# Performance work log

Measured on AMD Instinct MI355X. Metric: run time of the kernel, lower is better.

The kernel has to match this reference:

```python
import jax, jax.numpy as jnp
import numpy as np

B, T1, T2 = 2, 1024, 512
D_MODEL, N_HEAD, D_HEAD = 1024, 16, 64
SCALE = 1.0 / D_HEAD ** 0.5
EPS = 1e-5


def _skew(qe):
    # qe: [B, H, T, 2T-1] -> [B, H, T, T] via Transformer-XL pad/reshape trick
    b, h, t, x = qe.shape
    qe = jnp.pad(qe, ((0, 0), (0, 0), (0, 0), (0, 1))).reshape(b, h, 2 * t * t)
    qe = jnp.pad(qe, ((0, 0), (0, 0), (0, t - 1))).reshape(b, h, t + 1, 2 * t - 1)
    return qe[:, :, :t, -t:]


def setup_inputs() -> dict:
    key = jax.random.key(0)
    ks = jax.random.split(key, 12)
    s = 0.02
    return {
        "Q": jax.random.normal(ks[0], (B, T1, D_MODEL), jnp.float32),
        "K": jax.random.normal(ks[1], (B, T1, D_MODEL), jnp.float32),
        "V": jax.random.normal(ks[2], (B, T1, D_MODEL), jnp.float32),
        "lookup_table": jax.random.normal(ks[3], (2 * T1 - 1, D_HEAD), jnp.float32) * s,
        "valid_frames": jnp.sort(jax.random.randint(ks[4], (T2,), 0, T1)),
        "mask": jax.random.bernoulli(ks[5], 0.1, (B, N_HEAD, T1, T2)),
        "Wq": jax.random.normal(ks[6], (D_MODEL, N_HEAD * D_HEAD), jnp.float32) * s,
        "Wk": jax.random.normal(ks[7], (D_MODEL, N_HEAD * D_HEAD), jnp.float32) * s,
        "Wv": jax.random.normal(ks[8], (D_MODEL, N_HEAD * D_HEAD), jnp.float32) * s,
        "Wo": jax.random.normal(ks[9], (N_HEAD * D_HEAD, D_MODEL), jnp.float32) * s,
        "bo": jnp.zeros((D_MODEL,), jnp.float32),
        "ln_g": jnp.ones((D_MODEL,), jnp.float32),
        "ln_b": jnp.zeros((D_MODEL,), jnp.float32),
    }


def reference(Q, K, V, lookup_table, valid_frames, mask, Wq, Wk, Wv, Wo, bo, ln_g, ln_b):
    # gather valid KV frames (raw inputs, before projection)
    K = K[:, valid_frames]  # [B, T2, D]
    V = V[:, valid_frames]
    # pre-layernorm on Q only
    mu = jnp.mean(Q, axis=-1, keepdims=True)
    var = jnp.var(Q, axis=-1, keepdims=True)
    Qn = (Q - mu) * jax.lax.rsqrt(var + EPS) * ln_g + ln_b
    # projections -> [B, H, T, d_head]
    q = (Qn @ Wq).reshape(B, T1, N_HEAD, D_HEAD).transpose(0, 2, 1, 3)
    k = (K @ Wk).reshape(B, T2, N_HEAD, D_HEAD).transpose(0, 2, 1, 3)
    v = (V @ Wv).reshape(B, T2, N_HEAD, D_HEAD).transpose(0, 2, 1, 3)
    # content score + skewed relative-position score
    score = jnp.einsum("bhqd,bhkd->bhqk", q, k)  # [B,H,T1,T2]
    rel = jnp.einsum("bhqd,xd->bhqx", q, lookup_table)  # [B,H,T1,2T1-1]
    rel = _skew(rel)[:, :, :, valid_frames]  # [B,H,T1,T2]
    score = (score + rel) * SCALE
    score = jnp.where(mask, -jnp.finfo(score.dtype).max, score)
    attn = jax.nn.softmax(score, axis=-1)
    ctx = jnp.einsum("bhqk,bhkd->bhqd", attn, v)
    ctx = ctx.transpose(0, 2, 1, 3).reshape(B, T1, N_HEAD * D_HEAD)
    out = ctx @ Wo + bo  # dropout is identity at inference
    return out + ctx  # pre_layernorm=True branch
```

## Files before the change

### kernel.cpp

```cpp
#include <hip/hip_runtime.h>
#include <stdint.h>
#include <stddef.h>

typedef __attribute__((ext_vector_type(8))) short s16x8;
typedef __attribute__((ext_vector_type(4))) short s16x4;
typedef __attribute__((ext_vector_type(4))) float f32x4;

#define MFMA(a,b,c) __builtin_amdgcn_mfma_f32_16x16x32_bf16((a),(b),(c),0,0,0)

static __device__ __forceinline__ unsigned short f2b(float f){
  unsigned int b = __float_as_uint(f);
  b = (b + 0x7FFFu + ((b>>16)&1u)) >> 16;
  return (unsigned short)b;
}
static __device__ __forceinline__ float b2f(unsigned short u){
  return __uint_as_float(((unsigned int)u)<<16);
}


__global__ __launch_bounds__(256) void k_mask(const unsigned char* __restrict__ m,
    unsigned int* __restrict__ MB){
  const int t = threadIdx.x;
  const size_t g0 = (size_t)blockIdx.x*16;
  __shared__ int cnt1, cnt23;
  if(t==0){ cnt1=0; cnt23=0; }
  __syncthreads();
  const uint4* bp = (const uint4*)(m + g0*512);
  int l1=0,l23=0;
  #pragma unroll
  for(int i=0;i<2;i++){
    uint4 v = bp[t + i*256];
    unsigned int ws[4] = {v.x,v.y,v.z,v.w};
    #pragma unroll
    for(int j=0;j<4;j++){
      if((ws[j]>>8)&0xFFu) l1++;
      if(ws[j]>>16)        l23++;
    }
  }
  #pragma unroll
  for(int o=1;o<64;o<<=1){ l1 += __shfl_xor(l1,o); l23 += __shfl_xor(l23,o); }
  if((t&63)==0){ atomicAdd(&cnt1,l1); atomicAdd(&cnt23,l23); }
  __syncthreads();
  const int flag = cnt1 ? 1 : (cnt23 ? 2 : 0);

  const int rl = t>>4, f = t&15;
  const size_t base = (g0 + rl)*512 + f;
  unsigned int word = 0;
  if(flag==0){
    const int* p = (const int*)m;
    #pragma unroll
    for(int i=0;i<32;i++) word |= (p[base+i*16]!=0 ? 1u:0u) << i;
  } else if(flag==1){
    #pragma unroll
    for(int i=0;i<32;i++) word |= (m[base+i*16]!=0 ? 1u:0u) << i;
  } else {
    const float* p = (const float*)m;
    #pragma unroll
    for(int i=0;i<32;i++) word |= (p[base+i*16]!=0.f ? 1u:0u) << i;
  }
  MB[((size_t)blockIdx.x*4 + (t>>6))*64 + f*4 + (rl&3)] = word;
}

__global__ __launch_bounds__(256) void k_prep(
    const float* __restrict__ Q, const float* __restrict__ g, const float* __restrict__ be,
    unsigned short* __restrict__ Qn,
    const float* __restrict__ K, const float* __restrict__ V, const int* __restrict__ vf,
    unsigned short* __restrict__ Kg, unsigned short* __restrict__ Vg,
    const float* __restrict__ L, unsigned short* __restrict__ Lb,
    const float* __restrict__ W0, const float* __restrict__ W1,
    const float* __restrict__ W2, const float* __restrict__ W3,
    unsigned short* __restrict__ D0, unsigned short* __restrict__ D1,
    unsigned short* __restrict__ D2, unsigned short* __restrict__ D3){
  __shared__ float tile[64][65];
  __shared__ float red[8];
  const int bid = blockIdx.x, t = threadIdx.x;
  if(bid < 2048){
    const float4* xp = (const float4*)(Q + (size_t)bid*1024);
    float4 v = xp[t];
    float s  = v.x+v.y+v.z+v.w;
    float s2 = v.x*v.x+v.y*v.y+v.z*v.z+v.w*v.w;
    #pragma unroll
    for(int o=1;o<64;o<<=1){ s += __shfl_xor(s,o); s2 += __shfl_xor(s2,o); }
    int w = t>>6, l = t&63;
    if(l==0){ red[w]=s; red[4+w]=s2; }
    __syncthreads();
    s  = red[0]+red[1]+red[2]+red[3];
    s2 = red[4]+red[5]+red[6]+red[7];
    float mu = s*(1.f/1024.f);
    float var = s2*(1.f/1024.f) - mu*mu;
    float rs = rsqrtf(var + 1e-5f);
    float4 gv = ((const float4*)g)[t];
    float4 bv = ((const float4*)be)[t];
    ushort4 o4;
    o4.x = f2b((v.x-mu)*rs*gv.x + bv.x);
    o4.y = f2b((v.y-mu)*rs*gv.y + bv.y);
    o4.z = f2b((v.z-mu)*rs*gv.z + bv.z);
    o4.w = f2b((v.w-mu)*rs*gv.w + bv.w);
    ((ushort4*)(Qn + (size_t)bid*1024))[t] = o4;
  } else if(bid < 4096){
    int row = bid - 2048;
    int isV = row>>10, r = row&1023;
    int b = r>>9, jj = r&511;
    const float* src = (isV? V : K) + ((size_t)(b*1024 + vf[jj]))*1024;
    unsigned short* dst = (isV? Vg : Kg) + (size_t)r*1024;
    float4 v = ((const float4*)src)[t];
    ushort4 o; o.x=f2b(v.x); o.y=f2b(v.y); o.z=f2b(v.z); o.w=f2b(v.w);
    ((ushort4*)dst)[t] = o;
  } else if(bid < 4608){
    int i = (bid-4096)*256 + t;
    if(i < 2047*64) Lb[i] = f2b(L[i]);
  } else {
    int idx = bid - 4608;
    int z = idx>>8, rem = idx&255;
    int k0 = (rem&15)*64, n0 = (rem>>4)*64;
    const float* S = z==0?W0: z==1?W1: z==2?W2:W3;
    unsigned short* D = z==0?D0: z==1?D1: z==2?D2:D3;
    int tr = t>>6, tc = t&63;
    #pragma unroll
    for(int it=0;it<16;it++){ int r = it*4+tr; tile[r][tc] = S[(size_t)(k0+r)*1024 + n0+tc]; }
    __syncthreads();
    #pragma unroll
    for(int it=0;it<16;it++){ int r = it*4+tr; D[(size_t)(n0+r)*1024 + k0+tc] = f2b(tile[tc][r]); }
  }
}

__global__ __launch_bounds__(256) void k_proj(
    const short* __restrict__ QN, const short* __restrict__ WQT,
    const short* __restrict__ KG, const short* __restrict__ WKT,
    const short* __restrict__ WVT, const short* __restrict__ VG,
    unsigned short* __restrict__ QB, unsigned short* __restrict__ KB,
    unsigned short* __restrict__ VT){
  __shared__ __align__(16) short Ab[128*32];
  __shared__ __align__(16) short Bb[128*32];
  int bid = blockIdx.x;
  int mode, bx;
  if(bid<128){ mode=0; bx=bid>>3; }
  else if(bid<192){ mode=1; bx=(bid-128)>>3; }
  else { mode=2; bx=(bid-192)>>3; }
  int by = bid&7;
  const short* A  = mode==0? QN : mode==1? KG : WVT;
  const short* Bt = mode==0? WQT: mode==1? WKT: VG;

  const int t = threadIdx.x;
  const int w = t>>6, l = t&63;
  const int wr = w>>1, wc = w&1;
  const int fl15 = l&15, fl4 = l>>4;
  const size_t m0 = (size_t)bx*128, n0 = (size_t)by*128;
  const int srow = t>>2, scb = t&3;
  const int sg = scb ^ ((srow>>1)&3);
  const short* Ap = A + (m0+srow)*1024 + 8*sg;
  const short* Bp = Bt + (n0+srow)*1024 + 8*sg;

  f32x4 acc[4][4];
  const f32x4 zero = {0.f,0.f,0.f,0.f};
  #pragma unroll
  for(int m=0;m<4;m++)
    #pragma unroll
    for(int n=0;n<4;n++) acc[m][n] = zero;

  for(int k0=0;k0<1024;k0+=32){
    s16x8 a0 = *(const s16x8*)(Ap + k0);
    s16x8 a1 = *(const s16x8*)(Ap + 64*1024 + k0);
    s16x8 b0 = *(const s16x8*)(Bp + k0);
    s16x8 b1 = *(const s16x8*)(Bp + 64*1024 + k0);
    __syncthreads();
    *(s16x8*)(Ab + srow*32 + scb*8)      = a0;
    *(s16x8*)(Ab + (64+srow)*32 + scb*8) = a1;
    *(s16x8*)(Bb + srow*32 + scb*8)      = b0;
    *(s16x8*)(Bb + (64+srow)*32 + scb*8) = b1;
    __syncthreads();
    s16x8 af[4], bff[4];
    #pragma unroll
    for(int m=0;m<4;m++){
      int row = wr*64 + m*16 + fl15;
      int gg = fl4 ^ ((row>>1)&3);
      af[m] = *(const s16x8*)(Ab + row*32 + gg*8);
    }
    #pragma unroll
    for(int n=0;n<4;n++){
      int row = wc*64 + n*16 + fl15;
      int gg = fl4 ^ ((row>>1)&3);
      bff[n] = *(const s16x8*)(Bb + row*32 + gg*8);
    }
    #pragma unroll
    for(int m=0;m<4;m++)
      #pragma unroll
      for(int n=0;n<4;n++)
        acc[m][n] = MFMA(af[m], bff[n], acc[m][n]);
  }

  #pragma unroll
  for(int m=0;m<4;m++){
    #pragma unroll
    for(int n=0;n<4;n++){
      int mgb = (int)m0 + wr*64 + m*16 + 4*fl4;
      int ng  = (int)n0 + wc*64 + n*16 + fl15;
      #pragma unroll
      for(int p=0;p<4;p++){
        int mg = mgb + p;
        float v = acc[m][n][p];
        if(mode==0){ int b=mg>>10, i=mg&1023, h=ng>>6, d=ng&63;
          QB[((size_t)((b*16+h)*1024+i))*64 + d] = f2b(v); }
        else if(mode==1){ int b=mg>>9, jj=mg&511, h=ng>>6, d=ng&63;
          KB[((size_t)((b*16+h)*512+jj))*64 + d] = f2b(v); }
        else { int h=mg>>6, d=mg&63, b=ng>>9, jj=ng&511;
          VT[((size_t)((b*16+h)*64+d))*512 + jj] = f2b(v); }
      }
    }
  }
}

__global__ __launch_bounds__(256) void k_gemmO(
    const short* __restrict__ A, const short* __restrict__ Bt,
    float* __restrict__ out, const float* __restrict__ bo,
    const float* __restrict__ ctxf){
  __shared__ __align__(16) short Ab[128*32];
  __shared__ __align__(16) short Bb[128*32];
  const int t = threadIdx.x;
  const int w = t>>6, l = t&63;
  const int wr = w>>1, wc = w&1;
  const int fl15 = l&15, fl4 = l>>4;
  const size_t m0 = (size_t)blockIdx.x*128, n0 = (size_t)blockIdx.y*128;
  const int srow = t>>2, scb = t&3;
  const int sg = scb ^ ((srow>>1)&3);
  const short* Ap = A + (m0+srow)*1024 + 8*sg;
  const short* Bp = Bt + (n0+srow)*1024 + 8*sg;

  f32x4 acc[4][4];
  const f32x4 zero = {0.f,0.f,0.f,0.f};
  #pragma unroll
  for(int m=0;m<4;m++)
    #pragma unroll
    for(int n=0;n<4;n++) acc[m][n] = zero;

  for(int k0=0;k0<1024;k0+=32){
    s16x8 a0 = *(const s16x8*)(Ap + k0);
    s16x8 a1 = *(const s16x8*)(Ap + 64*1024 + k0);
    s16x8 b0 = *(const s16x8*)(Bp + k0);
    s16x8 b1 = *(const s16x8*)(Bp + 64*1024 + k0);
    __syncthreads();
    *(s16x8*)(Ab + srow*32 + scb*8)      = a0;
    *(s16x8*)(Ab + (64+srow)*32 + scb*8) = a1;
    *(s16x8*)(Bb + srow*32 + scb*8)      = b0;
    *(s16x8*)(Bb + (64+srow)*32 + scb*8) = b1;
    __syncthreads();
    s16x8 af[4], bff[4];
    #pragma unroll
    for(int m=0;m<4;m++){
      int row = wr*64 + m*16 + fl15;
      int gg = fl4 ^ ((row>>1)&3);
      af[m] = *(const s16x8*)(Ab + row*32 + gg*8);
    }
    #pragma unroll
    for(int n=0;n<4;n++){
      int row = wc*64 + n*16 + fl15;
      int gg = fl4 ^ ((row>>1)&3);
      bff[n] = *(const s16x8*)(Bb + row*32 + gg*8);
    }
    #pragma unroll
    for(int m=0;m<4;m++)
      #pragma unroll
      for(int n=0;n<4;n++)
        acc[m][n] = MFMA(af[m], bff[n], acc[m][n]);
  }

  #pragma unroll
  for(int m=0;m<4;m++){
    #pragma unroll
    for(int n=0;n<4;n++){
      int mgb = (int)m0 + wr*64 + m*16 + 4*fl4;
      int ng  = (int)n0 + wc*64 + n*16 + fl15;
      #pragma unroll
      for(int p=0;p<4;p++){
        int mg = mgb + p;
        size_t idx = (size_t)mg*1024 + ng;
        out[idx] = acc[m][n][p] + bo[ng] + ctxf[idx];
      }
    }
  }
}

#define RCH 256
#define RGS 288
__global__ __launch_bounds__(256) void k_rel(const short* __restrict__ qb,
    const short* __restrict__ lbf, const int* __restrict__ vf,
    unsigned short* __restrict__ relg){
  __shared__ __align__(16) short Gs[4][RGS*16];
  __shared__ int vfs[512];
  const int t=threadIdx.x, w=t>>6, l=t&63, fl15=l&15, fl4=l>>4;
  const int bh = blockIdx.x >> 6;
  const int qg = blockIdx.x & 63;
  const int qw = qg*16;
  for(int i=t;i<512;i+=256) vfs[i]=vf[i];
  __syncthreads();
  const int x0  = 1008 + vfs[0] - qw;
  const int xcw = x0 + w*RCH;
  const short* qp = qb + ((size_t)(bh*1024 + qw + fl15))*64 + 8*fl4;
  s16x8 qa0 = *(const s16x8*)qp;
  s16x8 qa1 = *(const s16x8*)(qp+32);
  short* Gw = &Gs[w][0];
  const f32x4 zero = {0.f,0.f,0.f,0.f};

  #pragma unroll 4
  for(int tt=0;tt<17;tt++){
    int xr = xcw + tt*16 + fl15; if(xr>2046) xr = 2046;
    const short* lp = lbf + (size_t)xr*64 + 8*fl4;
    s16x8 b0 = *(const s16x8*)lp;
    s16x8 b1 = *(const s16x8*)(lp+32);
    f32x4 a = zero;
    a = MFMA(qa0,b0,a); a = MFMA(qa1,b1,a);
    int cb = tt*16 + fl15 + 4*fl4;
    #pragma unroll
    for(int p=0;p<4;p++) Gw[(cb+p)*16 + 4*fl4 + p] = (short)f2b(a[p]);
  }

  unsigned short* rb = relg + ((size_t)(bh*64+qg))*32*256 + l*4;
  #pragma unroll 4
  for(int tt=0;tt<32;tt++){
    int jj = tt*16 + fl15;
    int o  = vfs[jj] - vfs[0] - RCH*w;
    if(o>=0 && o<RCH){
      s16x4 v4 = *(const s16x4*)(Gw + (o+15)*16 + 4*fl4);
      *(s16x4*)(rb + (size_t)tt*256) = v4;
    }
  }
}

__global__ __launch_bounds__(256,2) void k_attn(const short* __restrict__ qb,
    const short* __restrict__ kb, const short* __restrict__ vt,
    const short* __restrict__ relg, const unsigned int* __restrict__ MB,
    unsigned short* __restrict__ ctxb, float* __restrict__ ctxf){
  __shared__ __align__(16) short PB[4][1024];
  const int t=threadIdx.x, w=t>>6, l=t&63, fl15=l&15, fl4=l>>4;
  const int bh = blockIdx.y;
  const int qt = blockIdx.x;
  const int qw = qt*64 + w*16;
  const int qg = qt*4 + w;
  short* Pw = &PB[w][0];

  const int rowgrp = bh*256 + qt*16 + w*4 + fl4;
  uint4 mv = ((const uint4*)MB)[rowgrp*16 + fl15];
  unsigned int mbits[4] = {mv.x, mv.y, mv.z, mv.w};

  const short* qp = qb + ((size_t)(bh*1024 + qw + fl15))*64 + 8*fl4;
  s16x8 qa0 = *(const s16x8*)qp;
  s16x8 qa1 = *(const s16x8*)(qp+32);

  const short* kp_row = kb + ((size_t)(bh*512 + fl15))*64 + 8*fl4;
  const short* rp     = relg + ((size_t)(bh*64+qg))*32*256 + l*4;
  const short* vp[4];
  #pragma unroll
  for(int dt=0;dt<4;dt++) vp[dt] = vt + ((size_t)(bh*64 + dt*16 + fl15))*512 + 8*fl4;

  const f32x4 zero = {0.f,0.f,0.f,0.f};
  f32x4 facc[4];
  #pragma unroll
  for(int dt=0;dt<4;dt++) facc[dt] = zero;
  float m_run[4] = {-1e30f,-1e30f,-1e30f,-1e30f};
  float ps[4]    = {0.f,0.f,0.f,0.f};

  s16x8 kf[2][8];
  s16x4 rf[2][4];
  #pragma unroll
  for(int tl=0;tl<4;tl++){
    const short* ka = kp_row + (size_t)tl*1024;
    kf[0][2*tl]   = *(const s16x8*)ka;
    kf[0][2*tl+1] = *(const s16x8*)(ka+32);
    rf[0][tl]     = *(const s16x4*)(rp + tl*256);
  }

  #pragma unroll
  for(int c=0;c<8;c++){
    const int cur = c&1, nxt = cur^1;
    if(c<7){
      #pragma unroll
      for(int tl=0;tl<4;tl++){
        const short* ka = kp_row + (size_t)(4*(c+1)+tl)*1024;
        kf[nxt][2*tl]   = *(const s16x8*)ka;
        kf[nxt][2*tl+1] = *(const s16x8*)(ka+32);
        rf[nxt][tl]     = *(const s16x4*)(rp + (size_t)(4*(c+1)+tl)*256);
      }
    }
    s16x8 vfr[8];
    #pragma unroll
    for(int dt=0;dt<4;dt++){
      vfr[2*dt]   = *(const s16x8*)(vp[dt] + c*64);
      vfr[2*dt+1] = *(const s16x8*)(vp[dt] + c*64 + 32);
    }

    f32x4 S[4];
    #pragma unroll
    for(int tl=0;tl<4;tl++){
      f32x4 a = zero;
      a = MFMA(qa0, kf[cur][2*tl], a);
      a = MFMA(qa1, kf[cur][2*tl+1], a);
      #pragma unroll
      for(int p=0;p<4;p++){
        float sv = (a[p] + b2f((unsigned short)rf[cur][tl][p])) * 0.125f;
        bool mskb = (mbits[p]>>(4*c+tl))&1u;
        a[p] = mskb ? -1e30f : sv;
      }
      S[tl] = a;
    }

    float cm[4];
    #pragma unroll
    for(int p=0;p<4;p++){
      cm[p] = fmaxf(fmaxf(S[0][p],S[1][p]), fmaxf(S[2][p],S[3][p]));
      #pragma unroll
      for(int o=1;o<16;o<<=1) cm[p] = fmaxf(cm[p], __shfl_xor(cm[p],o));
      float mn = fmaxf(m_run[p], cm[p]);
      float fac = __expf(m_run[p]-mn);
      m_run[p] = mn;
      ps[p] *= fac;
      #pragma unroll
      for(int dt=0;dt<4;dt++) facc[dt][p] *= fac;
    }

    #pragma unroll
    for(int tl=0;tl<4;tl++){
      #pragma unroll
      for(int p=0;p<4;p++){
        float e = __expf(S[tl][p]-m_run[p]);
        ps[p] += e;
        int row = 4*fl4+p;
        Pw[row*64 + ((tl*16 + fl15) ^ (fl4<<4))] = (short)f2b(e);
      }
    }

    #pragma unroll
    for(int s=0;s<2;s++){
      s16x8 pa = *(const s16x8*)(Pw + fl15*64 + ((s*32 + fl4*8) ^ ((fl15>>2)<<4)));
      #pragma unroll
      for(int dt=0;dt<4;dt++)
        facc[dt] = MFMA(pa, vfr[2*dt+s], facc[dt]);
    }
  }

  float inv[4];
  #pragma unroll
  for(int p=0;p<4;p++){
    float sm = ps[p];
    #pragma unroll
    for(int o=1;o<16;o<<=1) sm += __shfl_xor(sm,o);
    inv[p] = 1.f/sm;
  }
  const int b = bh>>4, h = bh&15;
  const int irow0 = qw + 4*fl4;
  #pragma unroll
  for(int dt=0;dt<4;dt++){
    #pragma unroll
    for(int p=0;p<4;p++){
      float val = facc[dt][p] * inv[p];
      size_t idx = ((size_t)(b*1024 + irow0 + p))*1024 + h*64 + dt*16 + fl15;
      ctxb[idx] = f2b(val);
      ctxf[idx] = val;
    }
  }
}

extern "C" void kernel_launch(void* const* d_in, const int* in_sizes, int n_in,
                              void* d_out, int out_size, void* d_ws, size_t ws_size,
                              hipStream_t stream){
  (void)in_sizes; (void)n_in; (void)out_size; (void)ws_size;
  const float* Q  = (const float*)d_in[0];
  const float* K  = (const float*)d_in[1];
  const float* V  = (const float*)d_in[2];
  const float* Lt = (const float*)d_in[3];
  const int*   vf = (const int*)d_in[4];
  const void*  mk = d_in[5];
  const float* Wq = (const float*)d_in[6];
  const float* Wk = (const float*)d_in[7];
  const float* Wv = (const float*)d_in[8];
  const float* Wo = (const float*)d_in[9];
  const float* bo = (const float*)d_in[10];
  const float* lg = (const float*)d_in[11];
  const float* lb = (const float*)d_in[12];

  char* base = (char*)d_ws;
  size_t off = 0;
  auto alloc = [&](size_t bytes)->char*{
    char* p = base + off; off += (bytes + 255) & ~(size_t)255; return p; };
  unsigned int*   MBp = (unsigned int*)alloc(32768ull*16*4);
  unsigned short* QN  = (unsigned short*)alloc(2048ull*1024*2);
  unsigned short* KG  = (unsigned short*)alloc(1024ull*1024*2);
  unsigned short* VG  = (unsigned short*)alloc(1024ull*1024*2);
  unsigned short* WQT = (unsigned short*)alloc(1024ull*1024*2);
  unsigned short* WKT = (unsigned short*)alloc(1024ull*1024*2);
  unsigned short* WVT = (unsigned short*)alloc(1024ull*1024*2);
  unsigned short* WOT = (unsigned short*)alloc(1024ull*1024*2);
  unsigned short* LB  = (unsigned short*)alloc(2047ull*64*2);
  unsigned short* QB  = (unsigned short*)alloc(32ull*1024*64*2);
  unsigned short* KB  = (unsigned short*)alloc(32ull*512*64*2);
  unsigned short* VT  = (unsigned short*)alloc(32ull*64*512*2);
  unsigned short* RG  = (unsigned short*)alloc(32ull*64*32*256*2);
  unsigned short* CB  = (unsigned short*)alloc(2048ull*1024*2);
  float*          CF  = (float*)alloc(2048ull*1024*4);

  k_mask<<<2048,256,0,stream>>>((const unsigned char*)mk, MBp);
  k_prep<<<5632,256,0,stream>>>(Q, lg, lb, QN, K, V, vf, KG, VG, Lt, LB,
                                Wq, Wk, Wv, Wo, WQT, WKT, WVT, WOT);
  k_proj<<<256,256,0,stream>>>((const short*)QN,(const short*)WQT,
                               (const short*)KG,(const short*)WKT,
                               (const short*)WVT,(const short*)VG,
                               QB, KB, VT);
  k_rel<<<2048,256,0,stream>>>((const short*)QB,(const short*)LB, vf, RG);
  k_attn<<<dim3(16,32),256,0,stream>>>((const short*)QB,(const short*)KB,(const short*)VT,
                                       (const short*)RG, MBp, CB, CF);
  k_gemmO<<<dim3(16,8),256,0,stream>>>((const short*)CB,(const short*)WOT,
                                       (float*)d_out, bo, CF);
}
```

Measured before the change: 149.5 us.

## Fuse relative-position scores into attention kernel with split-KV across waves

Merges the relative-position kernel into the attention kernel: each block computes the skewed relative-score tile into shared memory and reads the gathered entries directly, removing the global relg buffer round-trip and one launch. The work split changes so each block handles 16 query rows and each of its four waves takes a quarter of the keys. Partial softmax statistics and outputs are then merged through shared memory. The trade-offs are 4x more blocks, extra barriers, a shared-memory reduction, and dropping the register double-buffering of K loads.

```diff
diff --git a/kernel.cpp b/kernel.cpp
--- a/kernel.cpp
+++ b/kernel.cpp
@@ -280,27 +280,32 @@
   }
 }
 
-#define RCH 256
-#define RGS 288
-__global__ __launch_bounds__(256) void k_rel(const short* __restrict__ qb,
+#define RGS 20
+#define GROWS 287
+__global__ __launch_bounds__(256,2) void k_attn(const short* __restrict__ qb,
+    const short* __restrict__ kb, const short* __restrict__ vt,
     const short* __restrict__ lbf, const int* __restrict__ vf,
-    unsigned short* __restrict__ relg){
-  __shared__ __align__(16) short Gs[4][RGS*16];
+    const unsigned int* __restrict__ MB,
+    unsigned short* __restrict__ ctxb, float* __restrict__ ctxf){
+  __shared__ __align__(16) short Gs[4][GROWS*RGS];
+  __shared__ __align__(16) short PB[4][1024];
   __shared__ int vfs[512];
   const int t=threadIdx.x, w=t>>6, l=t&63, fl15=l&15, fl4=l>>4;
-  const int bh = blockIdx.x >> 6;
-  const int qg = blockIdx.x & 63;
+  const int bh = blockIdx.y;
+  const int qg = blockIdx.x;
   const int qw = qg*16;
   for(int i=t;i<512;i+=256) vfs[i]=vf[i];
   __syncthreads();
-  const int x0  = 1008 + vfs[0] - qw;
-  const int xcw = x0 + w*RCH;
+  const int vf0 = vfs[0];
+  const int x0  = 1008 + vf0 - qw;
+  const int xcw = x0 + w*256;
+
   const short* qp = qb + ((size_t)(bh*1024 + qw + fl15))*64 + 8*fl4;
   s16x8 qa0 = *(const s16x8*)qp;
   s16x8 qa1 = *(const s16x8*)(qp+32);
+
   short* Gw = &Gs[w][0];
   const f32x4 zero = {0.f,0.f,0.f,0.f};
-
   #pragma unroll 4
   for(int tt=0;tt<17;tt++){
     int xr = xcw + tt*16 + fl15; if(xr>2046) xr = 2046;
@@ -311,98 +316,55 @@
     a = MFMA(qa0,b0,a); a = MFMA(qa1,b1,a);
     int cb = tt*16 + fl15 + 4*fl4;
     #pragma unroll
-    for(int p=0;p<4;p++) Gw[(cb+p)*16 + 4*fl4 + p] = (short)f2b(a[p]);
-  }
-
-  unsigned short* rb = relg + ((size_t)(bh*64+qg))*32*256 + l*4;
-  #pragma unroll 4
-  for(int tt=0;tt<32;tt++){
-    int jj = tt*16 + fl15;
-    int o  = vfs[jj] - vfs[0] - RCH*w;
-    if(o>=0 && o<RCH){
-      s16x4 v4 = *(const s16x4*)(Gw + (o+15)*16 + 4*fl4);
-      *(s16x4*)(rb + (size_t)tt*256) = v4;
-    }
-  }
-}
-
-__global__ __launch_bounds__(256,2) void k_attn(const short* __restrict__ qb,
-    const short* __restrict__ kb, const short* __restrict__ vt,
-    const short* __restrict__ relg, const unsigned int* __restrict__ MB,
-    unsigned short* __restrict__ ctxb, float* __restrict__ ctxf){
-  __shared__ __align__(16) short PB[4][1024];
-  const int t=threadIdx.x, w=t>>6, l=t&63, fl15=l&15, fl4=l>>4;
-  const int bh = blockIdx.y;
-  const int qt = blockIdx.x;
-  const int qw = qt*64 + w*16;
-  const int qg = qt*4 + w;
-  short* Pw = &PB[w][0];
-
-  const int rowgrp = bh*256 + qt*16 + w*4 + fl4;
+    for(int p=0;p<4;p++) Gw[(cb+p)*RGS + 4*fl4 + p] = (short)f2b(a[p]);
+  }
+
+  const int rowgrp = bh*256 + qg*4 + fl4;
   uint4 mv = ((const uint4*)MB)[rowgrp*16 + fl15];
   unsigned int mbits[4] = {mv.x, mv.y, mv.z, mv.w};
 
-  const short* qp = qb + ((size_t)(bh*1024 + qw + fl15))*64 + 8*fl4;
-  s16x8 qa0 = *(const s16x8*)qp;
-  s16x8 qa1 = *(const s16x8*)(qp+32);
+  __syncthreads();
 
   const short* kp_row = kb + ((size_t)(bh*512 + fl15))*64 + 8*fl4;
-  const short* rp     = relg + ((size_t)(bh*64+qg))*32*256 + l*4;
-  const short* vp[4];
-  #pragma unroll
-  for(int dt=0;dt<4;dt++) vp[dt] = vt + ((size_t)(bh*64 + dt*16 + fl15))*512 + 8*fl4;
-
-  const f32x4 zero = {0.f,0.f,0.f,0.f};
+  const short* vpb[4];
+  #pragma unroll
+  for(int dt=0;dt<4;dt++)
+    vpb[dt] = vt + ((size_t)(bh*64 + dt*16 + fl15))*512 + w*128 + 8*fl4;
+
   f32x4 facc[4];
   #pragma unroll
   for(int dt=0;dt<4;dt++) facc[dt] = zero;
   float m_run[4] = {-1e30f,-1e30f,-1e30f,-1e30f};
   float ps[4]    = {0.f,0.f,0.f,0.f};
-
-  s16x8 kf[2][8];
-  s16x4 rf[2][4];
-  #pragma unroll
-  for(int tl=0;tl<4;tl++){
-    const short* ka = kp_row + (size_t)tl*1024;
-    kf[0][2*tl]   = *(const s16x8*)ka;
-    kf[0][2*tl+1] = *(const s16x8*)(ka+32);
-    rf[0][tl]     = *(const s16x4*)(rp + tl*256);
-  }
-
-  #pragma unroll
-  for(int c=0;c<8;c++){
-    const int cur = c&1, nxt = cur^1;
-    if(c<7){
-      #pragma unroll
-      for(int tl=0;tl<4;tl++){
-        const short* ka = kp_row + (size_t)(4*(c+1)+tl)*1024;
-        kf[nxt][2*tl]   = *(const s16x8*)ka;
-        kf[nxt][2*tl+1] = *(const s16x8*)(ka+32);
-        rf[nxt][tl]     = *(const s16x4*)(rp + (size_t)(4*(c+1)+tl)*256);
-      }
-    }
+  short* Pw = &PB[w][0];
+
+  for(int c=0;c<2;c++){
     s16x8 vfr[8];
     #pragma unroll
     for(int dt=0;dt<4;dt++){
-      vfr[2*dt]   = *(const s16x8*)(vp[dt] + c*64);
-      vfr[2*dt+1] = *(const s16x8*)(vp[dt] + c*64 + 32);
-    }
-
+      vfr[2*dt]   = *(const s16x8*)(vpb[dt] + c*64);
+      vfr[2*dt+1] = *(const s16x8*)(vpb[dt] + c*64 + 32);
+    }
     f32x4 S[4];
     #pragma unroll
     for(int tl=0;tl<4;tl++){
+      int ttg = 8*w + 4*c + tl;
+      const short* ka = kp_row + (size_t)ttg*1024;
+      s16x8 k0v = *(const s16x8*)ka;
+      s16x8 k1v = *(const s16x8*)(ka+32);
       f32x4 a = zero;
-      a = MFMA(qa0, kf[cur][2*tl], a);
-      a = MFMA(qa1, kf[cur][2*tl+1], a);
+      a = MFMA(qa0,k0v,a); a = MFMA(qa1,k1v,a);
+      int jj = ttg*16 + fl15;
+      int o  = vfs[jj] - vf0;
+      s16x4 rl = *(const s16x4*)(&Gs[o>>8][((o&255)+15)*RGS + 4*fl4]);
       #pragma unroll
       for(int p=0;p<4;p++){
-        float sv = (a[p] + b2f((unsigned short)rf[cur][tl][p])) * 0.125f;
-        bool mskb = (mbits[p]>>(4*c+tl))&1u;
+        float sv = (a[p] + b2f((unsigned short)rl[p])) * 0.125f;
+        bool mskb = (mbits[p]>>ttg)&1u;
         a[p] = mskb ? -1e30f : sv;
       }
       S[tl] = a;
     }
-
     float cm[4];
     #pragma unroll
     for(int p=0;p<4;p++){
@@ -416,7 +378,6 @@
       #pragma unroll
       for(int dt=0;dt<4;dt++) facc[dt][p] *= fac;
     }
-
     #pragma unroll
     for(int tl=0;tl<4;tl++){
       #pragma unroll
@@ -427,7 +388,6 @@
         Pw[row*64 + ((tl*16 + fl15) ^ (fl4<<4))] = (short)f2b(e);
       }
     }
-
     #pragma unroll
     for(int s=0;s<2;s++){
       s16x8 pa = *(const s16x8*)(Pw + fl15*64 + ((s*32 + fl4*8) ^ ((fl15>>2)<<4)));
@@ -437,25 +397,45 @@
     }
   }
 
-  float inv[4];
   #pragma unroll
   for(int p=0;p<4;p++){
-    float sm = ps[p];
-    #pragma unroll
-    for(int o=1;o<16;o<<=1) sm += __shfl_xor(sm,o);
-    inv[p] = 1.f/sm;
-  }
+    #pragma unroll
+    for(int o=1;o<16;o<<=1) ps[p] += __shfl_xor(ps[p],o);
+  }
+
+  __syncthreads();
+  float* MT = (float*)&Gs[0][0];
+  float* ST = MT + 64;
+  float* MG = ST + 64;
+  if(fl15==0){
+    #pragma unroll
+    for(int p=0;p<4;p++){ MT[w*16 + 4*fl4+p] = m_run[p]; ST[w*16 + 4*fl4+p] = ps[p]; }
+  }
+  __syncthreads();
+  float scale[4];
+  #pragma unroll
+  for(int p=0;p<4;p++){
+    int row = 4*fl4+p;
+    float ms  = fmaxf(fmaxf(MT[row],MT[16+row]), fmaxf(MT[32+row],MT[48+row]));
+    float den = __expf(MT[row]-ms)*ST[row] + __expf(MT[16+row]-ms)*ST[16+row]
+              + __expf(MT[32+row]-ms)*ST[32+row] + __expf(MT[48+row]-ms)*ST[48+row];
+    scale[p] = __expf(m_run[p]-ms) / den;
+  }
+  #pragma unroll
+  for(int dt=0;dt<4;dt++)
+    #pragma unroll
+    for(int p=0;p<4;p++)
+      MG[(w*16 + 4*fl4+p)*65 + dt*16 + fl15] = facc[dt][p]*scale[p];
+  __syncthreads();
   const int b = bh>>4, h = bh&15;
-  const int irow0 = qw + 4*fl4;
-  #pragma unroll
-  for(int dt=0;dt<4;dt++){
-    #pragma unroll
-    for(int p=0;p<4;p++){
-      float val = facc[dt][p] * inv[p];
-      size_t idx = ((size_t)(b*1024 + irow0 + p))*1024 + h*64 + dt*16 + fl15;
-      ctxb[idx] = f2b(val);
-      ctxf[idx] = val;
-    }
+  #pragma unroll
+  for(int p=0;p<4;p++){
+    int row = 4*fl4+p;
+    float v = MG[(row)*65    + w*16+fl15] + MG[(16+row)*65 + w*16+fl15]
+            + MG[(32+row)*65 + w*16+fl15] + MG[(48+row)*65 + w*16+fl15];
+    size_t idx = ((size_t)(b*1024 + qw + row))*1024 + h*64 + w*16 + fl15;
+    ctxb[idx] = f2b(v);
+    ctxf[idx] = v;
   }
 }
 
@@ -493,7 +473,6 @@
   unsigned short* QB  = (unsigned short*)alloc(32ull*1024*64*2);
   unsigned short* KB  = (unsigned short*)alloc(32ull*512*64*2);
   unsigned short* VT  = (unsigned short*)alloc(32ull*64*512*2);
-  unsigned short* RG  = (unsigned short*)alloc(32ull*64*32*256*2);
   unsigned short* CB  = (unsigned short*)alloc(2048ull*1024*2);
   float*          CF  = (float*)alloc(2048ull*1024*4);
 
@@ -504,9 +483,8 @@
                                (const short*)KG,(const short*)WKT,
                                (const short*)WVT,(const short*)VG,
                                QB, KB, VT);
-  k_rel<<<2048,256,0,stream>>>((const short*)QB,(const short*)LB, vf, RG);
-  k_attn<<<dim3(16,32),256,0,stream>>>((const short*)QB,(const short*)KB,(const short*)VT,
-                                       (const short*)RG, MBp, CB, CF);
+  k_attn<<<dim3(64,32),256,0,stream>>>((const short*)QB,(const short*)KB,(const short*)VT,
+                                       (const short*)LB, vf, MBp, CB, CF);
   k_gemmO<<<dim3(16,8),256,0,stream>>>((const short*)CB,(const short*)WOT,
                                        (float*)d_out, bo, CF);
 }
```

Result: faster. 146.0 us (-2.4%).
